# Optimization experiments

Hardware: AMD Instinct MI355X
Metric: run time of the kernel (lower is better)

The kernel has to match this reference:

```python
import jax, jax.numpy as jnp
import numpy as np

_J6 = jnp.array([[0,0,0,0,0,1],[0,0,0,0,-1,0],[0,0,0,1,0,0],
                 [0,0,1,0,0,0],[0,-1,0,0,0,0],[1,0,0,0,0,0]], dtype=jnp.float32)
_PAIRS4 = [(0,1),(0,2),(0,3),(1,2),(1,3),(2,3)]
H = 16  # n_heads

def _ln(x, g, b, eps=1e-5):
    m = jnp.mean(x, axis=-1, keepdims=True)
    v = jnp.var(x, axis=-1, keepdims=True)
    return (x - m) / jnp.sqrt(v + eps) * g + b

def _exterior(p1, p2):
    # Plucker coordinates of the line through p1,p2 in R^4 -> R^6, normalized
    parts = [p1[..., i] * p2[..., j] - p1[..., j] * p2[..., i] for i, j in _PAIRS4]
    L = jnp.stack(parts, axis=-1)
    n = jnp.linalg.norm(L, axis=-1, keepdims=True)
    return L / jnp.maximum(n, 1e-12)

def _iterated_gram_attn(x, Wqkv, bqkv, W1w, W2w, W1r, W2r, Wmv, bmv, Wmg, bmg,
                        mem_scale, iter_mix, decay_logits, Wout, bout):
    B, T, D = x.shape
    dh = D // H
    # ---- standard causal attention branch ----
    qkv = (x @ Wqkv + bqkv).reshape(B, T, 3, H, dh)
    q = jnp.transpose(qkv[:, :, 0], (0, 2, 1, 3))  # bhtd
    k = jnp.transpose(qkv[:, :, 1], (0, 2, 1, 3))
    v = jnp.transpose(qkv[:, :, 2], (0, 2, 1, 3))
    scores = jnp.einsum('bhtd,bhsd->bhts', q, k) * (dh ** -0.5)
    causal = jnp.tril(jnp.ones((T, T), dtype=bool))
    scores = jnp.where(causal, scores, -jnp.inf)
    attn = jax.nn.softmax(scores, axis=-1)  # dropout is eval-mode identity
    seq_out = jnp.einsum('bhts,bhsd->bhtd', attn, v).transpose(0, 2, 1, 3).reshape(B, T, D)
    # ---- Gram memory branch ----
    x_prev = jnp.concatenate([jnp.zeros_like(x[:, :1]), x[:, :-1]], axis=1)
    w1 = (x_prev @ W1w).reshape(B, T, H, 4)
    w2 = (x @ W2w).reshape(B, T, H, 4)
    write_lines = _exterior(w1, w2)                       # (B,T,H,6)
    r1 = (x @ W1r).reshape(B, T, H, 4)
    r2 = (x @ W2r).reshape(B, T, H, 4)
    read_lines = _exterior(r1, r2)                        # (B,T,H,6)
    Jw = jnp.einsum('bthi,ij->bhtj', write_lines, _J6)    # (B,H,T,6)
    rd = jnp.transpose(read_lines, (0, 2, 1, 3))          # (B,H,T,6)
    decays = jax.nn.sigmoid(decay_logits)                 # (H,)
    pos = jnp.arange(T, dtype=x.dtype)
    outer = Jw[..., :, None] * Jw[..., None, :]           # (B,H,T,6,6)
    dinv = (1.0 / jnp.maximum(decays, 1e-6))[:, None] ** pos[None, :]  # (H,T)
    M = jnp.cumsum(outer * dinv[None, :, :, None, None], axis=2)
    M = jnp.concatenate([jnp.zeros_like(M[:, :, :1]), M[:, :, :-1]], axis=2)  # shift: strictly past
    dfwd = decays[:, None] ** pos[None, :]
    M = M * dfwd[None, :, :, None, None]                  # (B,H,T,6,6)
    rdM = jnp.einsum('bhti,bhtij->bhtj', rd, M)
    score_M = jnp.sum(rdM * rd, axis=-1)                  # (B,H,T)
    score_M2 = jnp.sum(rdM * rdM, axis=-1)
    alpha = jax.nn.sigmoid(iter_mix[0])
    mem_score = (1 - alpha) * score_M + alpha * score_M2
    mem_val = x @ Wmv + bmv                               # (B,T,D)
    gate = jax.nn.sigmoid(x @ Wmg + bmg)                  # (B,T,H)
    gated = jax.nn.sigmoid(jnp.transpose(mem_score, (0, 2, 1)) * mem_scale[None, None, :]) * gate
    gated = jnp.mean(gated, axis=-1, keepdims=True)       # (B,T,1)
    return (seq_out + gated * mem_val) @ Wout + bout

def _block(x, ln1_g, ln1_b, Wqkv, bqkv, W1w, W2w, W1r, W2r, Wmv, bmv, Wmg, bmg,
           mem_scale, iter_mix, decay_logits, Wout, bout,
           ln2_g, ln2_b, Wfc, bfc, Wproj, bproj):
    h = _ln(x, ln1_g, ln1_b)
    x = x + _iterated_gram_attn(h, Wqkv, bqkv, W1w, W2w, W1r, W2r, Wmv, bmv,
                                Wmg, bmg, mem_scale, iter_mix, decay_logits, Wout, bout)
    h2 = _ln(x, ln2_g, ln2_b)
    mlp = jax.nn.gelu(h2 @ Wfc + bfc, approximate=False) @ Wproj + bproj
    return x + mlp

def setup_inputs() -> dict:
    key = jax.random.key(0)
    B, T, D = 2, 1024, 1024
    dff = 4 * D
    ks = jax.random.split(key, 16)
    s = 0.02
    inp = {
        'x': jax.random.normal(ks[0], (B, T, D), jnp.float32),
        'ln1_g': jnp.ones((D,), jnp.float32), 'ln1_b': jnp.zeros((D,), jnp.float32),
        'Wqkv': jax.random.normal(ks[1], (D, 3 * D), jnp.float32) * s,
        'bqkv': jnp.zeros((3 * D,), jnp.float32),
        'W1w': jax.random.normal(ks[2], (D, 4 * H), jnp.float32) * s,
        'W2w': jax.random.normal(ks[3], (D, 4 * H), jnp.float32) * s,
        'W1r': jax.random.normal(ks[4], (D, 4 * H), jnp.float32) * s,
        'W2r': jax.random.normal(ks[5], (D, 4 * H), jnp.float32) * s,
        'Wmv': jax.random.normal(ks[6], (D, D), jnp.float32) * s,
        'bmv': jnp.zeros((D,), jnp.float32),
        'Wmg': jax.random.normal(ks[7], (D, H), jnp.float32) * s,
        'bmg': jnp.zeros((H,), jnp.float32),
        'mem_scale': jnp.full((H,), 0.1, jnp.float32),
        'iter_mix': jnp.zeros((1,), jnp.float32),
        'decay_logits': jnp.full((H,), 4.6, jnp.float32) + 0.1 * jax.random.normal(ks[8], (H,), jnp.float32),
        'Wout': jax.random.normal(ks[9], (D, D), jnp.float32) * s,
        'bout': jnp.zeros((D,), jnp.float32),
        'ln2_g': jnp.ones((D,), jnp.float32), 'ln2_b': jnp.zeros((D,), jnp.float32),
        'Wfc': jax.random.normal(ks[10], (D, dff), jnp.float32) * s,
        'bfc': jnp.zeros((dff,), jnp.float32),
        'Wproj': jax.random.normal(ks[11], (dff, D), jnp.float32) * s,
        'bproj': jnp.zeros((D,), jnp.float32),
    }
    return inp

def reference(x, ln1_g, ln1_b, Wqkv, bqkv, W1w, W2w, W1r, W2r, Wmv, bmv, Wmg, bmg,
              mem_scale, iter_mix, decay_logits, Wout, bout,
              ln2_g, ln2_b, Wfc, bfc, Wproj, bproj):
    return _block(x, ln1_g, ln1_b, Wqkv, bqkv, W1w, W2w, W1r, W2r, Wmv, bmv, Wmg, bmg,
                  mem_scale, iter_mix, decay_logits, Wout, bout,
                  ln2_g, ln2_b, Wfc, bfc, Wproj, bproj)
```

## Files before the change

### kernel.cpp

```cpp
#include <hip/hip_runtime.h>
#include <hip/hip_bf16.h>
#include <math.h>

typedef float f32x4 __attribute__((ext_vector_type(4)));
typedef _Float16 f16x8 __attribute__((ext_vector_type(8)));
typedef _Float16 f16x4 __attribute__((ext_vector_type(4)));

#define TT 1024
#define DD 1024
#define QS 4608

typedef __attribute__((address_space(1))) const void gas_void;
typedef __attribute__((address_space(3))) void las_void;
static __device__ __forceinline__ void gl_lds16(const void* g, void* l) {
  __builtin_amdgcn_global_load_lds((gas_void*)g, (las_void*)l, 16, 0, 0);
}

__global__ __launch_bounds__(512) void gemm_t16(
    const _Float16* __restrict__ A, const _Float16* __restrict__ Wt,
    const float* __restrict__ bias, void* __restrict__ Cv,
    int N, int K, int act, int gx, int mode, int ktiles) {
  __shared__ __align__(16) _Float16 As[3][128 * 32];
  __shared__ __align__(16) _Float16 Bs[3][128 * 32];
  const int tid = threadIdx.x;
  const int lane = tid & 63;
  const int wid = tid >> 6;
  const int wr = wid >> 1, wc = wid & 1;
  const int g = lane >> 4, l16 = lane & 15;
  const int cpx = gridDim.x >> 3;
  const int wg = (blockIdx.x & 7) * cpx + (blockIdx.x >> 3);
  const int row0 = (wg / gx) * 128, col0 = (wg % gx) * 128;
  const int kbeg = blockIdx.y * ktiles * 32;

  f32x4 acc[2][4];
#pragma unroll
  for (int m = 0; m < 2; ++m)
#pragma unroll
    for (int n = 0; n < 4; ++n) acc[m][n] = (f32x4){0.f, 0.f, 0.f, 0.f};

  const int srow = tid >> 2;
  const int goff = ((tid & 3) ^ ((srow >> 1) & 3)) << 3;
  const _Float16* agp = A + (size_t)(row0 + srow) * K + kbeg + goff;
  const _Float16* bgp = Wt + (size_t)(col0 + srow) * K + kbeg + goff;
  const int ldst = tid * 16;

  const int prm = (l16 >> 1) & 3;

  gl_lds16(agp, (char*)As[0] + ldst);
  gl_lds16(bgp, (char*)Bs[0] + ldst);
  if (1 < ktiles) {
    gl_lds16(agp + 32, (char*)As[1] + ldst);
    gl_lds16(bgp + 32, (char*)Bs[1] + ldst);
  }

  int cs = 0, ss = 2;
  for (int kt = 0; kt < ktiles; ++kt) {
    if (kt < ktiles - 1) asm volatile("s_waitcnt vmcnt(2)" ::: "memory");
    else                 asm volatile("s_waitcnt vmcnt(0)" ::: "memory");
    __builtin_amdgcn_s_barrier();
    __builtin_amdgcn_sched_barrier(0);
    if (kt + 2 < ktiles) {
      const int kp = (kt + 2) * 32;
      gl_lds16(agp + kp, (char*)As[ss] + ldst);
      gl_lds16(bgp + kp, (char*)Bs[ss] + ldst);
    }
    f16x8 af[2], bf[4];
#pragma unroll
    for (int m = 0; m < 2; ++m) {
      const int r = wr * 32 + m * 16 + l16;
      af[m] = *(const f16x8*)(As[cs] + r * 32 + ((g ^ prm) << 3));
    }
#pragma unroll
    for (int n = 0; n < 4; ++n) {
      const int r = wc * 64 + n * 16 + l16;
      bf[n] = *(const f16x8*)(Bs[cs] + r * 32 + ((g ^ prm) << 3));
    }
#pragma unroll
    for (int m = 0; m < 2; ++m)
#pragma unroll
      for (int n = 0; n < 4; ++n)
        acc[m][n] = __builtin_amdgcn_mfma_f32_16x16x32_f16(af[m], bf[n], acc[m][n], 0, 0, 0);
    cs = (cs == 2) ? 0 : cs + 1;
    ss = (ss == 2) ? 0 : ss + 1;
  }
#pragma unroll
  for (int m = 0; m < 2; ++m) {
#pragma unroll
    for (int n = 0; n < 4; ++n) {
      const int col = col0 + wc * 64 + n * 16 + l16;
      const float bv = (mode != 2 && bias) ? bias[col] : 0.f;
#pragma unroll
      for (int rg = 0; rg < 4; ++rg) {
        const int row = row0 + wr * 32 + m * 16 + g * 4 + rg;
        const size_t off = (size_t)row * N + col;
        float v = acc[m][n][rg] + bv;
        if (act == 1) v = 0.5f * v * (1.f + erff(v * 0.70710678118654752f));
        if (mode == 2) atomicAdd(&((float*)Cv)[off], v);
        else ((_Float16*)Cv)[off] = (_Float16)v;
      }
    }
  }
}

__global__ __launch_bounds__(256) void transT(const float* __restrict__ W,
                                              _Float16* __restrict__ WT, int K, int N) {
  __shared__ float tile[64][65];
  const int n0 = blockIdx.x * 64, k0 = blockIdx.y * 64;
  const int tn = threadIdx.x & 63, tk4 = threadIdx.x >> 6;
#pragma unroll
  for (int it = 0; it < 16; ++it) {
    const int k = k0 + it * 4 + tk4;
    tile[tn][it * 4 + tk4] = W[(size_t)k * N + n0 + tn];
  }
  __syncthreads();
  const int on = threadIdx.x >> 2, ok = threadIdx.x & 3;
  f16x8 a, b;
#pragma unroll
  for (int j = 0; j < 8; ++j) {
    a[j] = (_Float16)tile[on][ok * 16 + j];
    b[j] = (_Float16)tile[on][ok * 16 + 8 + j];
  }
  _Float16* dst = WT + (size_t)(n0 + on) * K + k0 + ok * 16;
  *(f16x8*)dst = a;
  *(f16x8*)(dst + 8) = b;
}

__global__ __launch_bounds__(256) void prep_megaT(
    const float* __restrict__ Wqkv, const float* __restrict__ W1w, const float* __restrict__ W2w,
    const float* __restrict__ W1r, const float* __restrict__ W2r, const float* __restrict__ Wmg,
    const float* __restrict__ Wmv, _Float16* __restrict__ WmT) {
  __shared__ float tile[64][65];
  const int n0 = blockIdx.x * 64, k0 = blockIdx.y * 64;
  const int tn = threadIdx.x & 63, tk4 = threadIdx.x >> 6;
#pragma unroll
  for (int it = 0; it < 16; ++it) {
    const int k = k0 + it * 4 + tk4;
    const int n = n0 + tn;
    float v;
    if (n < 3072) v = Wqkv[(size_t)k * 3072 + n];
    else if (n < 3136) v = W1w[k * 64 + n - 3072];
    else if (n < 3200) v = W2w[k * 64 + n - 3136];
    else if (n < 3264) v = W1r[k * 64 + n - 3200];
    else if (n < 3328) v = W2r[k * 64 + n - 3264];
    else if (n < 3344) v = Wmg[k * 16 + n - 3328];
    else if (n < 3584) v = 0.f;
    else v = Wmv[(size_t)k * 1024 + n - 3584];
    tile[tn][it * 4 + tk4] = v;
  }
  __syncthreads();
  const int on = threadIdx.x >> 2, ok = threadIdx.x & 3;
  f16x8 a, b;
#pragma unroll
  for (int j = 0; j < 8; ++j) {
    a[j] = (_Float16)tile[on][ok * 16 + j];
    b[j] = (_Float16)tile[on][ok * 16 + 8 + j];
  }
  _Float16* dst = WmT + (size_t)(n0 + on) * 1024 + k0 + ok * 16;
  *(f16x8*)dst = a;
  *(f16x8*)(dst + 8) = b;
}

__global__ void bm_init(const float* __restrict__ bqkv, const float* __restrict__ bmg,
                        const float* __restrict__ bmv, float* __restrict__ bm) {
  const int col = blockIdx.x * 256 + threadIdx.x;
  if (col >= 4608) return;
  float b = 0.f;
  if (col < 3072) b = bqkv[col];
  else if (col >= 3328 && col < 3344) b = bmg[col - 3328];
  else if (col >= 3584) b = bmv[col - 3584];
  bm[col] = b;
}

__global__ __launch_bounds__(256) void ln16(const float* __restrict__ in,
    const float* __restrict__ gw, const float* __restrict__ bw, _Float16* __restrict__ out) {
  const int row = blockIdx.x, tid = threadIdx.x;
  const float* x = in + (size_t)row * DD;
  const float4 v = *(const float4*)(x + tid * 4);
  float s = v.x + v.y + v.z + v.w;
  float sq = v.x * v.x + v.y * v.y + v.z * v.z + v.w * v.w;
#pragma unroll
  for (int off = 32; off >= 1; off >>= 1) { s += __shfl_xor(s, off); sq += __shfl_xor(sq, off); }
  __shared__ float red[8];
  const int lane = tid & 63, wv = tid >> 6;
  if (lane == 0) { red[wv] = s; red[4 + wv] = sq; }
  __syncthreads();
  s = red[0] + red[1] + red[2] + red[3];
  sq = red[4] + red[5] + red[6] + red[7];
  const float mean = s * (1.f / 1024.f);
  const float var = sq * (1.f / 1024.f) - mean * mean;
  const float rstd = rsqrtf(var + 1e-5f);
  const float4 g4 = *(const float4*)(gw + tid * 4);
  const float4 b4 = *(const float4*)(bw + tid * 4);
  f16x4 o;
  o[0] = (_Float16)((v.x - mean) * rstd * g4.x + b4.x);
  o[1] = (_Float16)((v.y - mean) * rstd * g4.y + b4.y);
  o[2] = (_Float16)((v.z - mean) * rstd * g4.z + b4.z);
  o[3] = (_Float16)((v.w - mean) * rstd * g4.w + b4.w);
  *(f16x4*)(out + (size_t)row * DD + tid * 4) = o;
}

static __device__ __forceinline__ int swzA(int row, int k) {
  return row * 64 + ((((k >> 3) ^ row) & 7) << 3) + (k & 7);
}
static __device__ __forceinline__ int swzV(int row, int k) {
  return row * 64 + ((((k >> 3) ^ row ^ (row >> 3)) & 7) << 3) + (k & 7);
}

__global__ __launch_bounds__(256) void attn_mfma(const _Float16* __restrict__ qkv,
                                                 _Float16* __restrict__ seq_out) {
  __shared__ __align__(16) _Float16 Kl[64 * 64];
  __shared__ __align__(16) _Float16 Vt[64 * 64];
  __shared__ __align__(16) _Float16 Pl[4][16 * 64];
  const int tid = threadIdx.x, lane = tid & 63, wq = tid >> 6;
  const int g = lane >> 4, l16 = lane & 15;
  const int qt = blockIdx.x, hh = blockIdx.y, bb = blockIdx.z;
  const int nt = qt + 1;

  f16x8 qf[2];
  {
    const _Float16* qp = qkv + (size_t)(bb * TT + qt * 64 + wq * 16 + l16) * QS + hh * 64;
#pragma unroll
    for (int ks = 0; ks < 2; ++ks) {
      const f16x8 a = *(const f16x8*)(qp + ks * 32 + g * 8);
#pragma unroll
      for (int j = 0; j < 8; ++j) qf[ks][j] = (_Float16)((float)a[j] * 0.125f);
    }
  }

  f32x4 oacc[4];
#pragma unroll
  for (int n = 0; n < 4; ++n) oacc[n] = (f32x4){0.f, 0.f, 0.f, 0.f};
  float m[4] = {-INFINITY, -INFINITY, -INFINITY, -INFINITY};
  float l[4] = {0.f, 0.f, 0.f, 0.f};

  const int skey = tid >> 2, sc4 = tid & 3;

  for (int tt = 0; tt < nt; ++tt) {
    if (tt) __syncthreads();
    {
      const _Float16* kp = qkv + (size_t)(bb * TT + tt * 64 + skey) * QS + hh * 64 + 1024;
      const _Float16* vp = kp + 1024;
#pragma unroll
      for (int ii = 0; ii < 4; ++ii) {
        const int d0 = sc4 * 4 + ii * 16;
        *(f16x4*)(Kl + swzA(skey, d0)) = *(const f16x4*)(kp + d0);
        const f16x4 vv = *(const f16x4*)(vp + d0);
        Vt[swzV(d0 + 0, skey)] = vv[0];
        Vt[swzV(d0 + 1, skey)] = vv[1];
        Vt[swzV(d0 + 2, skey)] = vv[2];
        Vt[swzV(d0 + 3, skey)] = vv[3];
      }
    }
    __syncthreads();
    f32x4 s[4];
#pragma unroll
    for (int n = 0; n < 4; ++n) s[n] = (f32x4){0.f, 0.f, 0.f, 0.f};
#pragma unroll
    for (int ks = 0; ks < 2; ++ks) {
      f16x8 kf[4];
#pragma unroll
      for (int n = 0; n < 4; ++n) kf[n] = *(const f16x8*)(Kl + swzA(n * 16 + l16, ks * 32 + g * 8));
#pragma unroll
      for (int n = 0; n < 4; ++n)
        s[n] = __builtin_amdgcn_mfma_f32_16x16x32_f16(qf[ks], kf[n], s[n], 0, 0, 0);
    }
    if (tt == qt) {
      const int rloc = wq * 16 + g * 4;
#pragma unroll
      for (int n = 0; n < 4; ++n) {
        const int cloc = n * 16 + l16;
#pragma unroll
        for (int reg = 0; reg < 4; ++reg)
          if (cloc > rloc + reg) s[n][reg] = -INFINITY;
      }
    }
    float f[4];
#pragma unroll
    for (int reg = 0; reg < 4; ++reg) {
      float t = fmaxf(fmaxf(s[0][reg], s[1][reg]), fmaxf(s[2][reg], s[3][reg]));
#pragma unroll
      for (int off = 1; off < 16; off <<= 1) t = fmaxf(t, __shfl_xor(t, off));
      const float nm = fmaxf(m[reg], t);
      f[reg] = __expf(m[reg] - nm);
      m[reg] = nm;
    }
    float rs[4] = {0.f, 0.f, 0.f, 0.f};
#pragma unroll
    for (int n = 0; n < 4; ++n) {
#pragma unroll
      for (int reg = 0; reg < 4; ++reg) {
        const float p = __expf(s[n][reg] - m[reg]);
        rs[reg] += p;
        Pl[wq][swzA(g * 4 + reg, n * 16 + l16)] = (_Float16)p;
      }
    }
#pragma unroll
    for (int reg = 0; reg < 4; ++reg) {
      float t = rs[reg];
#pragma unroll
      for (int off = 1; off < 16; off <<= 1) t += __shfl_xor(t, off);
      l[reg] = l[reg] * f[reg] + t;
    }
#pragma unroll
    for (int n = 0; n < 4; ++n)
#pragma unroll
      for (int reg = 0; reg < 4; ++reg) oacc[n][reg] *= f[reg];
#pragma unroll
    for (int ks = 0; ks < 2; ++ks) {
      const f16x8 pa = *(const f16x8*)(Pl[wq] + swzA(l16, ks * 32 + g * 8));
      f16x8 vb[4];
#pragma unroll
      for (int n = 0; n < 4; ++n) vb[n] = *(const f16x8*)(Vt + swzV(n * 16 + l16, ks * 32 + g * 8));
#pragma unroll
      for (int n = 0; n < 4; ++n)
        oacc[n] = __builtin_amdgcn_mfma_f32_16x16x32_f16(pa, vb[n], oacc[n], 0, 0, 0);
    }
  }
#pragma unroll
  for (int n = 0; n < 4; ++n) {
#pragma unroll
    for (int reg = 0; reg < 4; ++reg) {
      const int r = qt * 64 + wq * 16 + g * 4 + reg;
      seq_out[(size_t)(bb * TT + r) * DD + hh * 64 + n * 16 + l16] = (_Float16)(oacc[n][reg] / l[reg]);
    }
  }
}

static __device__ __forceinline__ void ext6(const float* a, const float* b, float* L) {
  L[0] = a[0] * b[1] - a[1] * b[0];
  L[1] = a[0] * b[2] - a[2] * b[0];
  L[2] = a[0] * b[3] - a[3] * b[0];
  L[3] = a[1] * b[2] - a[2] * b[1];
  L[4] = a[1] * b[3] - a[3] * b[1];
  L[5] = a[2] * b[3] - a[3] * b[2];
  const float n = sqrtf(L[0]*L[0] + L[1]*L[1] + L[2]*L[2] + L[3]*L[3] + L[4]*L[4] + L[5]*L[5]);
  const float s = 1.f / fmaxf(n, 1e-12f);
#pragma unroll
  for (int i = 0; i < 6; ++i) L[i] *= s;
}

__global__ void lines_post(const _Float16* __restrict__ mega, float* __restrict__ jw,
                           float* __restrict__ rdv, float* __restrict__ gate) {
  const int idx = blockIdx.x * 256 + threadIdx.x;
  const int h = idx & 15;
  const int bt = idx >> 4;
  const int t = bt & 1023;
  const int b = bt >> 10;
  const _Float16* row = mega + (size_t)bt * QS + 3072;
  float w1[4] = {0.f, 0.f, 0.f, 0.f}, w2[4], r1[4], r2[4];
  if (t > 0) {
#pragma unroll
    for (int i = 0; i < 4; ++i) w1[i] = (float)row[-QS + h * 4 + i];
  }
#pragma unroll
  for (int i = 0; i < 4; ++i) {
    w2[i] = (float)row[64 + h * 4 + i];
    r1[i] = (float)row[128 + h * 4 + i];
    r2[i] = (float)row[192 + h * 4 + i];
  }
  const float gp = (float)row[256 + h];
  float wl[6], rl[6];
  ext6(w1, w2, wl);
  ext6(r1, r2, rl);
  const size_t o = ((size_t)(b * 16 + h) * 1024 + t) * 6;
  jw[o + 0] =  wl[5]; jw[o + 1] = -wl[4]; jw[o + 2] =  wl[3];
  jw[o + 3] =  wl[2]; jw[o + 4] = -wl[1]; jw[o + 5] =  wl[0];
#pragma unroll
  for (int i = 0; i < 6; ++i) rdv[o + i] = rl[i];
  gate[idx] = 1.f / (1.f + __expf(-gp));
}

static __device__ __forceinline__ int midx(int i, int j) {
  return (i <= j) ? (i * (13 - i)) / 2 + (j - i) : (j * (13 - j)) / 2 + (i - j);
}

__global__ __launch_bounds__(64) void gram_scan(const float* __restrict__ jwv,
    const float* __restrict__ rdv, const float* __restrict__ decay_logits,
    const float* __restrict__ iter_mix, float* __restrict__ mem_score) {
  const int h = blockIdx.x & 15, b = blockIdx.x >> 4;
  const int lane = threadIdx.x;
  const float decay = 1.f / (1.f + __expf(-decay_logits[h]));
  const float alpha = 1.f / (1.f + __expf(-iter_mix[0]));
  __shared__ float sd[64 * 193];
  const size_t base = (size_t)(b * 16 + h) * 1024 * 6;
  for (int it = 0; it < 96; ++it) {
    const int idx = it * 64 + lane;
    const int t = idx / 6, i = idx - 6 * t;
    const int ld = t >> 4, s = t & 15;
    sd[ld * 193 + s * 6 + i] = jwv[base + idx];
    sd[ld * 193 + 96 + s * 6 + i] = rdv[base + idx];
  }
  __syncthreads();
  const float* seg = sd + lane * 193;

  float C[21];
#pragma unroll
  for (int e = 0; e < 21; ++e) C[e] = 0.f;
  for (int s = 0; s < 16; ++s) {
    float J[6], dJ[6];
#pragma unroll
    for (int i = 0; i < 6; ++i) { J[i] = seg[s * 6 + i]; dJ[i] = decay * J[i]; }
#pragma unroll
    for (int i = 0; i < 6; ++i)
#pragma unroll
      for (int j = i; j < 6; ++j)
        C[midx(i, j)] = decay * C[midx(i, j)] + dJ[i] * J[j];
  }
  const float d2 = decay * decay, d4 = d2 * d2, d8 = d4 * d4;
  float fk = d8 * d8;
#pragma unroll
  for (int k = 0; k < 6; ++k) {
    const int off = 1 << k;
#pragma unroll
    for (int e = 0; e < 21; ++e) {
      const float u = __shfl(C[e], lane - off);
      if (lane >= off) C[e] += fk * u;
    }
    fk = fk * fk;
  }
  float M[21];
#pragma unroll
  for (int e = 0; e < 21; ++e) {
    const float u = __shfl(C[e], lane - 1);
    M[e] = (lane >= 1) ? u : 0.f;
  }
  float* msp = mem_score + (size_t)(b * 16 + h) * 1024 + lane * 16;
  for (int s = 0; s < 16; ++s) {
    float J[6], r[6];
#pragma unroll
    for (int i = 0; i < 6; ++i) { J[i] = seg[s * 6 + i]; r[i] = seg[96 + s * 6 + i]; }
    float rdM[6];
#pragma unroll
    for (int i = 0; i < 6; ++i) {
      float a = 0.f;
#pragma unroll
      for (int j = 0; j < 6; ++j) a += M[midx(i, j)] * r[j];
      rdM[i] = a;
    }
    float s1 = 0.f, s2 = 0.f;
#pragma unroll
    for (int i = 0; i < 6; ++i) { s1 += rdM[i] * r[i]; s2 += rdM[i] * rdM[i]; }
    msp[s] = (1.f - alpha) * s1 + alpha * s2;
    float dJ[6];
#pragma unroll
    for (int i = 0; i < 6; ++i) dJ[i] = decay * J[i];
#pragma unroll
    for (int i = 0; i < 6; ++i)
#pragma unroll
      for (int j = i; j < 6; ++j)
        M[midx(i, j)] = decay * M[midx(i, j)] + dJ[i] * J[j];
  }
}

__global__ __launch_bounds__(256) void combine_kernel(const _Float16* __restrict__ seq,
    const _Float16* __restrict__ mega, const float* __restrict__ ms,
    const float* __restrict__ gate, const float* __restrict__ mem_scale,
    _Float16* __restrict__ outp) {
  const int bt = blockIdx.x;
  const int b = bt >> 10, t = bt & 1023;
  __shared__ float hterm[16];
  const int tid = threadIdx.x;
  if (tid < 16) {
    const float sc = ms[(size_t)(b * 16 + tid) * 1024 + t];
    const float gt = gate[(size_t)bt * 16 + tid];
    hterm[tid] = (1.f / (1.f + __expf(-sc * mem_scale[tid]))) * gt;
  }
  __syncthreads();
  float acc = 0.f;
#pragma unroll
  for (int h = 0; h < 16; ++h) acc += hterm[h];
  const float g = acc * (1.f / 16.f);
  const f16x4 s4 = *(const f16x4*)(seq + (size_t)bt * 1024 + tid * 4);
  const f16x4 m4 = *(const f16x4*)(mega + (size_t)bt * QS + 3584 + tid * 4);
  f16x4 o;
#pragma unroll
  for (int j = 0; j < 4; ++j) o[j] = (_Float16)((float)s4[j] + g * (float)m4[j]);
  *(f16x4*)(outp + (size_t)bt * 1024 + tid * 4) = o;
}

__global__ void addb_init(const float* __restrict__ src, const float* __restrict__ bias,
                          float* __restrict__ dst) {
  const size_t i = (size_t)blockIdx.x * 256 + threadIdx.x;
  const int c4 = (int)(i & 255);
  const float4 s = ((const float4*)src)[i];
  const float4 b = ((const float4*)bias)[c4];
  float4 o;
  o.x = s.x + b.x; o.y = s.y + b.y; o.z = s.z + b.z; o.w = s.w + b.w;
  ((float4*)dst)[i] = o;
}

extern "C" void kernel_launch(void* const* d_in, const int* in_sizes, int n_in,
                              void* d_out, int out_size, void* d_ws, size_t ws_size,
                              hipStream_t stream) {
  (void)in_sizes; (void)n_in; (void)out_size; (void)ws_size;
  const float* x       = (const float*)d_in[0];
  const float* ln1_g   = (const float*)d_in[1];
  const float* ln1_b   = (const float*)d_in[2];
  const float* Wqkv    = (const float*)d_in[3];
  const float* bqkv    = (const float*)d_in[4];
  const float* W1w     = (const float*)d_in[5];
  const float* W2w     = (const float*)d_in[6];
  const float* W1r     = (const float*)d_in[7];
  const float* W2r     = (const float*)d_in[8];
  const float* Wmv     = (const float*)d_in[9];
  const float* bmv     = (const float*)d_in[10];
  const float* Wmg     = (const float*)d_in[11];
  const float* bmg     = (const float*)d_in[12];
  const float* mscale  = (const float*)d_in[13];
  const float* itermix = (const float*)d_in[14];
  const float* dlogits = (const float*)d_in[15];
  const float* Wout    = (const float*)d_in[16];
  const float* bout    = (const float*)d_in[17];
  const float* ln2_g   = (const float*)d_in[18];
  const float* ln2_b   = (const float*)d_in[19];
  const float* Wfc     = (const float*)d_in[20];
  const float* bfc     = (const float*)d_in[21];
  const float* Wproj   = (const float*)d_in[22];
  const float* bproj   = (const float*)d_in[23];
  float* out = (float*)d_out;
  float* ws = (float*)d_ws;

  const size_t M1 = 1u << 20;
  _Float16* h16    = (_Float16*)ws;
  _Float16* WmT    = (_Float16*)(ws + 1 * M1);
  float*    bm     = ws + 3407872;
  float*    jw     = ws + 3538944;
  float*    rd     = ws + 3538944 + 196608;
  float*    gate   = ws + 3538944 + 393216;
  float*    ms     = ws + 3538944 + 425984;
  float*    y      = ws + 4 * M1;
  _Float16* mega   = (_Float16*)(ws + 6 * M1);
  _Float16* fc16   = (_Float16*)(ws + 6 * M1);
  _Float16* seq16  = (_Float16*)(ws + 11010048);
  _Float16* WoutT  = (_Float16*)(ws + 12058624);
  _Float16* WfcT   = (_Float16*)(ws + 12 * M1);
  _Float16* WprojT = (_Float16*)(ws + 14 * M1);

  prep_megaT<<<dim3(72, 16), 256, 0, stream>>>(Wqkv, W1w, W2w, W1r, W2r, Wmg, Wmv, WmT);
  bm_init<<<18, 256, 0, stream>>>(bqkv, bmg, bmv, bm);
  transT<<<dim3(16, 16), 256, 0, stream>>>(Wout, WoutT, 1024, 1024);
  transT<<<dim3(64, 16), 256, 0, stream>>>(Wfc, WfcT, 1024, 4096);
  transT<<<dim3(16, 64), 256, 0, stream>>>(Wproj, WprojT, 4096, 1024);

  ln16<<<2048, 256, 0, stream>>>(x, ln1_g, ln1_b, h16);
  gemm_t16<<<576, 512, 0, stream>>>(h16, WmT, bm, mega, 4608, 1024, 0, 36, 1, 32);
  attn_mfma<<<dim3(16, 16, 2), 256, 0, stream>>>(mega, seq16);
  lines_post<<<128, 256, 0, stream>>>(mega, jw, rd, gate);
  gram_scan<<<32, 64, 0, stream>>>(jw, rd, dlogits, itermix, ms);
  combine_kernel<<<2048, 256, 0, stream>>>(seq16, mega, ms, gate, mscale, h16);
  addb_init<<<2048, 256, 0, stream>>>(x, bout, y);
  gemm_t16<<<dim3(128, 4), 512, 0, stream>>>(h16, WoutT, nullptr, y, 1024, 1024, 0, 8, 2, 8);
  ln16<<<2048, 256, 0, stream>>>(y, ln2_g, ln2_b, h16);
  gemm_t16<<<512, 512, 0, stream>>>(h16, WfcT, bfc, fc16, 4096, 1024, 1, 32, 1, 32);
  addb_init<<<2048, 256, 0, stream>>>(y, bproj, out);
  gemm_t16<<<dim3(128, 4), 512, 0, stream>>>(fc16, WprojT, nullptr, out, 1024, 4096, 0, 8, 2, 32);
}
```

Baseline: 251.0 us.

## Merge weight-prep kernels, pair causal attention tiles, fuse residual into Wout GEMM

All weight transposes and the bias init are merged into a single prep_all launch, which cuts launch overhead. The attention kernel now gives each block two query tiles (p and 15-p) that share the K/V loads in shared memory, so per-block causal work is balanced and K/V traffic is reduced. The Wout projection no longer uses a split-K atomicAdd with a separate addb_init. It runs as one full-K GEMM with a mode that adds bias and residual in the epilogue and writes fp32 directly. In exchange the Wout GEMM has fewer blocks (128), and the attention grid is halved while each block does roughly twice the work.

```diff
diff --git a/kernel.cpp b/kernel.cpp
--- a/kernel.cpp
+++ b/kernel.cpp
@@ -18,10 +18,10 @@
 
 __global__ __launch_bounds__(512) void gemm_t16(
     const _Float16* __restrict__ A, const _Float16* __restrict__ Wt,
-    const float* __restrict__ bias, void* __restrict__ Cv,
-    int N, int K, int act, int gx, int mode, int ktiles) {
-  __shared__ __align__(16) _Float16 As[3][128 * 32];
-  __shared__ __align__(16) _Float16 Bs[3][128 * 32];
+    const float* __restrict__ bias, const float* __restrict__ residual,
+    void* __restrict__ Cv, int N, int K, int act, int gx, int mode, int ktiles) {
+  __shared__ __align__(16) _Float16 As[3][4096];
+  __shared__ __align__(16) _Float16 Bs[3][4096];
   const int tid = threadIdx.x;
   const int lane = tid & 63;
   const int wid = tid >> 6;
@@ -72,8 +72,8 @@
     }
 #pragma unroll
     for (int n = 0; n < 4; ++n) {
-      const int r = wc * 64 + n * 16 + l16;
-      bf[n] = *(const f16x8*)(Bs[cs] + r * 32 + ((g ^ prm) << 3));
+      const int c = wc * 64 + n * 16 + l16;
+      bf[n] = *(const f16x8*)(Bs[cs] + c * 32 + ((g ^ prm) << 3));
     }
 #pragma unroll
     for (int m = 0; m < 2; ++m)
@@ -96,24 +96,24 @@
         float v = acc[m][n][rg] + bv;
         if (act == 1) v = 0.5f * v * (1.f + erff(v * 0.70710678118654752f));
         if (mode == 2) atomicAdd(&((float*)Cv)[off], v);
+        else if (mode == 3) ((float*)Cv)[off] = v + residual[off];
         else ((_Float16*)Cv)[off] = (_Float16)v;
       }
     }
   }
 }
 
-__global__ __launch_bounds__(256) void transT(const float* __restrict__ W,
-                                              _Float16* __restrict__ WT, int K, int N) {
+static __device__ __forceinline__ void trans_tile(const float* __restrict__ W,
+    _Float16* __restrict__ WT, int K, int N, int n0, int k0, int tid) {
   __shared__ float tile[64][65];
-  const int n0 = blockIdx.x * 64, k0 = blockIdx.y * 64;
-  const int tn = threadIdx.x & 63, tk4 = threadIdx.x >> 6;
+  const int tn = tid & 63, tk4 = tid >> 6;
 #pragma unroll
   for (int it = 0; it < 16; ++it) {
     const int k = k0 + it * 4 + tk4;
     tile[tn][it * 4 + tk4] = W[(size_t)k * N + n0 + tn];
   }
   __syncthreads();
-  const int on = threadIdx.x >> 2, ok = threadIdx.x & 3;
+  const int on = tid >> 2, ok = tid & 3;
   f16x8 a, b;
 #pragma unroll
   for (int j = 0; j < 8; ++j) {
@@ -125,50 +125,64 @@
   *(f16x8*)(dst + 8) = b;
 }
 
-__global__ __launch_bounds__(256) void prep_megaT(
+__global__ __launch_bounds__(256) void prep_all(
     const float* __restrict__ Wqkv, const float* __restrict__ W1w, const float* __restrict__ W2w,
     const float* __restrict__ W1r, const float* __restrict__ W2r, const float* __restrict__ Wmg,
-    const float* __restrict__ Wmv, _Float16* __restrict__ WmT) {
-  __shared__ float tile[64][65];
-  const int n0 = blockIdx.x * 64, k0 = blockIdx.y * 64;
-  const int tn = threadIdx.x & 63, tk4 = threadIdx.x >> 6;
-#pragma unroll
-  for (int it = 0; it < 16; ++it) {
-    const int k = k0 + it * 4 + tk4;
-    const int n = n0 + tn;
-    float v;
-    if (n < 3072) v = Wqkv[(size_t)k * 3072 + n];
-    else if (n < 3136) v = W1w[k * 64 + n - 3072];
-    else if (n < 3200) v = W2w[k * 64 + n - 3136];
-    else if (n < 3264) v = W1r[k * 64 + n - 3200];
-    else if (n < 3328) v = W2r[k * 64 + n - 3264];
-    else if (n < 3344) v = Wmg[k * 16 + n - 3328];
-    else if (n < 3584) v = 0.f;
-    else v = Wmv[(size_t)k * 1024 + n - 3584];
-    tile[tn][it * 4 + tk4] = v;
-  }
-  __syncthreads();
-  const int on = threadIdx.x >> 2, ok = threadIdx.x & 3;
-  f16x8 a, b;
-#pragma unroll
-  for (int j = 0; j < 8; ++j) {
-    a[j] = (_Float16)tile[on][ok * 16 + j];
-    b[j] = (_Float16)tile[on][ok * 16 + 8 + j];
-  }
-  _Float16* dst = WmT + (size_t)(n0 + on) * 1024 + k0 + ok * 16;
-  *(f16x8*)dst = a;
-  *(f16x8*)(dst + 8) = b;
-}
-
-__global__ void bm_init(const float* __restrict__ bqkv, const float* __restrict__ bmg,
-                        const float* __restrict__ bmv, float* __restrict__ bm) {
-  const int col = blockIdx.x * 256 + threadIdx.x;
-  if (col >= 4608) return;
-  float b = 0.f;
-  if (col < 3072) b = bqkv[col];
-  else if (col >= 3328 && col < 3344) b = bmg[col - 3328];
-  else if (col >= 3584) b = bmv[col - 3584];
-  bm[col] = b;
+    const float* __restrict__ Wmv, const float* __restrict__ Wout, const float* __restrict__ Wfc,
+    const float* __restrict__ Wproj, const float* __restrict__ bqkv, const float* __restrict__ bmg,
+    const float* __restrict__ bmv, _Float16* __restrict__ WmT, _Float16* __restrict__ WoutT,
+    _Float16* __restrict__ WfcT, _Float16* __restrict__ WprojT, float* __restrict__ bm) {
+  const int id = blockIdx.x;
+  const int tid = threadIdx.x;
+  if (id < 1152) {
+    __shared__ float tile[64][65];
+    const int n0 = (id % 72) * 64, k0 = (id / 72) * 64;
+    const int tn = tid & 63, tk4 = tid >> 6;
+#pragma unroll
+    for (int it = 0; it < 16; ++it) {
+      const int k = k0 + it * 4 + tk4;
+      const int n = n0 + tn;
+      float v;
+      if (n < 3072) v = Wqkv[(size_t)k * 3072 + n];
+      else if (n < 3136) v = W1w[k * 64 + n - 3072];
+      else if (n < 3200) v = W2w[k * 64 + n - 3136];
+      else if (n < 3264) v = W1r[k * 64 + n - 3200];
+      else if (n < 3328) v = W2r[k * 64 + n - 3264];
+      else if (n < 3344) v = Wmg[k * 16 + n - 3328];
+      else if (n < 3584) v = 0.f;
+      else v = Wmv[(size_t)k * 1024 + n - 3584];
+      tile[tn][it * 4 + tk4] = v;
+    }
+    __syncthreads();
+    const int on = tid >> 2, ok = tid & 3;
+    f16x8 a, b;
+#pragma unroll
+    for (int j = 0; j < 8; ++j) {
+      a[j] = (_Float16)tile[on][ok * 16 + j];
+      b[j] = (_Float16)tile[on][ok * 16 + 8 + j];
+    }
+    _Float16* dst = WmT + (size_t)(n0 + on) * 1024 + k0 + ok * 16;
+    *(f16x8*)dst = a;
+    *(f16x8*)(dst + 8) = b;
+  } else if (id < 1408) {
+    const int i2 = id - 1152;
+    trans_tile(Wout, WoutT, 1024, 1024, (i2 % 16) * 64, (i2 / 16) * 64, tid);
+  } else if (id < 2432) {
+    const int i2 = id - 1408;
+    trans_tile(Wfc, WfcT, 1024, 4096, (i2 % 64) * 64, (i2 / 64) * 64, tid);
+  } else if (id < 3456) {
+    const int i2 = id - 2432;
+    trans_tile(Wproj, WprojT, 4096, 1024, (i2 % 16) * 64, (i2 / 16) * 64, tid);
+  } else {
+    const int col = (id - 3456) * 256 + tid;
+    if (col < 4608) {
+      float b = 0.f;
+      if (col < 3072) b = bqkv[col];
+      else if (col >= 3328 && col < 3344) b = bmg[col - 3328];
+      else if (col >= 3584) b = bmv[col - 3584];
+      bm[col] = b;
+    }
+  }
 }
 
 __global__ __launch_bounds__(256) void ln16(const float* __restrict__ in,
@@ -206,6 +220,75 @@
   return row * 64 + ((((k >> 3) ^ row ^ (row >> 3)) & 7) << 3) + (k & 7);
 }
 
+static __device__ __forceinline__ void attn_step(
+    const f16x8* qf, f32x4* oacc, float* m, float* l,
+    const _Float16* Kl, const _Float16* Vt, _Float16* Plw,
+    bool diag, int wq, int g, int l16) {
+  f32x4 s[4];
+#pragma unroll
+  for (int n = 0; n < 4; ++n) s[n] = (f32x4){0.f, 0.f, 0.f, 0.f};
+#pragma unroll
+  for (int ks = 0; ks < 2; ++ks) {
+    f16x8 kf[4];
+#pragma unroll
+    for (int n = 0; n < 4; ++n) kf[n] = *(const f16x8*)(Kl + swzA(n * 16 + l16, ks * 32 + g * 8));
+#pragma unroll
+    for (int n = 0; n < 4; ++n)
+      s[n] = __builtin_amdgcn_mfma_f32_16x16x32_f16(qf[ks], kf[n], s[n], 0, 0, 0);
+  }
+  if (diag) {
+    const int rloc = wq * 16 + g * 4;
+#pragma unroll
+    for (int n = 0; n < 4; ++n) {
+      const int cloc = n * 16 + l16;
+#pragma unroll
+      for (int reg = 0; reg < 4; ++reg)
+        if (cloc > rloc + reg) s[n][reg] = -INFINITY;
+    }
+  }
+  float f[4];
+#pragma unroll
+  for (int reg = 0; reg < 4; ++reg) {
+    float t = fmaxf(fmaxf(s[0][reg], s[1][reg]), fmaxf(s[2][reg], s[3][reg]));
+#pragma unroll
+    for (int off = 1; off < 16; off <<= 1) t = fmaxf(t, __shfl_xor(t, off));
+    const float nm = fmaxf(m[reg], t);
+    f[reg] = __expf(m[reg] - nm);
+    m[reg] = nm;
+  }
+  float rs[4] = {0.f, 0.f, 0.f, 0.f};
+#pragma unroll
+  for (int n = 0; n < 4; ++n) {
+#pragma unroll
+    for (int reg = 0; reg < 4; ++reg) {
+      const float p = __expf(s[n][reg] - m[reg]);
+      rs[reg] += p;
+      Plw[swzA(g * 4 + reg, n * 16 + l16)] = (_Float16)p;
+    }
+  }
+#pragma unroll
+  for (int reg = 0; reg < 4; ++reg) {
+    float t = rs[reg];
+#pragma unroll
+    for (int off = 1; off < 16; off <<= 1) t += __shfl_xor(t, off);
+    l[reg] = l[reg] * f[reg] + t;
+  }
+#pragma unroll
+  for (int n = 0; n < 4; ++n)
+#pragma unroll
+    for (int reg = 0; reg < 4; ++reg) oacc[n][reg] *= f[reg];
+#pragma unroll
+  for (int ks = 0; ks < 2; ++ks) {
+    const f16x8 pa = *(const f16x8*)(Plw + swzA(l16, ks * 32 + g * 8));
+    f16x8 vb[4];
+#pragma unroll
+    for (int n = 0; n < 4; ++n) vb[n] = *(const f16x8*)(Vt + swzV(n * 16 + l16, ks * 32 + g * 8));
+#pragma unroll
+    for (int n = 0; n < 4; ++n)
+      oacc[n] = __builtin_amdgcn_mfma_f32_16x16x32_f16(pa, vb[n], oacc[n], 0, 0, 0);
+  }
+}
+
 __global__ __launch_bounds__(256) void attn_mfma(const _Float16* __restrict__ qkv,
                                                  _Float16* __restrict__ seq_out) {
   __shared__ __align__(16) _Float16 Kl[64 * 64];
@@ -213,29 +296,40 @@
   __shared__ __align__(16) _Float16 Pl[4][16 * 64];
   const int tid = threadIdx.x, lane = tid & 63, wq = tid >> 6;
   const int g = lane >> 4, l16 = lane & 15;
-  const int qt = blockIdx.x, hh = blockIdx.y, bb = blockIdx.z;
-  const int nt = qt + 1;
-
-  f16x8 qf[2];
+  const int p = blockIdx.x, hh = blockIdx.y, bb = blockIdx.z;
+  const int qt0 = p, qt1 = 15 - p;
+  const int ntt = qt1 + 1;
+
+  f16x8 qf0[2], qf1[2];
   {
-    const _Float16* qp = qkv + (size_t)(bb * TT + qt * 64 + wq * 16 + l16) * QS + hh * 64;
+    const _Float16* q0 = qkv + (size_t)(bb * TT + qt0 * 64 + wq * 16 + l16) * QS + hh * 64;
+    const _Float16* q1 = qkv + (size_t)(bb * TT + qt1 * 64 + wq * 16 + l16) * QS + hh * 64;
 #pragma unroll
     for (int ks = 0; ks < 2; ++ks) {
-      const f16x8 a = *(const f16x8*)(qp + ks * 32 + g * 8);
-#pragma unroll
-      for (int j = 0; j < 8; ++j) qf[ks][j] = (_Float16)((float)a[j] * 0.125f);
-    }
-  }
-
-  f32x4 oacc[4];
-#pragma unroll
-  for (int n = 0; n < 4; ++n) oacc[n] = (f32x4){0.f, 0.f, 0.f, 0.f};
-  float m[4] = {-INFINITY, -INFINITY, -INFINITY, -INFINITY};
-  float l[4] = {0.f, 0.f, 0.f, 0.f};
+      const f16x8 a0 = *(const f16x8*)(q0 + ks * 32 + g * 8);
+      const f16x8 a1 = *(const f16x8*)(q1 + ks * 32 + g * 8);
+#pragma unroll
+      for (int j = 0; j < 8; ++j) {
+        qf0[ks][j] = (_Float16)((float)a0[j] * 0.125f);
+        qf1[ks][j] = (_Float16)((float)a1[j] * 0.125f);
+      }
+    }
+  }
+
+  f32x4 oacc0[4], oacc1[4];
+#pragma unroll
+  for (int n = 0; n < 4; ++n) {
+    oacc0[n] = (f32x4){0.f, 0.f, 0.f, 0.f};
+    oacc1[n] = (f32x4){0.f, 0.f, 0.f, 0.f};
+  }
+  float m0[4] = {-INFINITY, -INFINITY, -INFINITY, -INFINITY};
+  float l0[4] = {0.f, 0.f, 0.f, 0.f};
+  float m1[4] = {-INFINITY, -INFINITY, -INFINITY, -INFINITY};
+  float l1[4] = {0.f, 0.f, 0.f, 0.f};
 
   const int skey = tid >> 2, sc4 = tid & 3;
 
-  for (int tt = 0; tt < nt; ++tt) {
+  for (int tt = 0; tt < ntt; ++tt) {
     if (tt) __syncthreads();
     {
       const _Float16* kp = qkv + (size_t)(bb * TT + tt * 64 + skey) * QS + hh * 64 + 1024;
@@ -252,76 +346,18 @@
       }
     }
     __syncthreads();
-    f32x4 s[4];
-#pragma unroll
-    for (int n = 0; n < 4; ++n) s[n] = (f32x4){0.f, 0.f, 0.f, 0.f};
-#pragma unroll
-    for (int ks = 0; ks < 2; ++ks) {
-      f16x8 kf[4];
-#pragma unroll
-      for (int n = 0; n < 4; ++n) kf[n] = *(const f16x8*)(Kl + swzA(n * 16 + l16, ks * 32 + g * 8));
-#pragma unroll
-      for (int n = 0; n < 4; ++n)
-        s[n] = __builtin_amdgcn_mfma_f32_16x16x32_f16(qf[ks], kf[n], s[n], 0, 0, 0);
-    }
-    if (tt == qt) {
-      const int rloc = wq * 16 + g * 4;
-#pragma unroll
-      for (int n = 0; n < 4; ++n) {
-        const int cloc = n * 16 + l16;
-#pragma unroll
-        for (int reg = 0; reg < 4; ++reg)
-          if (cloc > rloc + reg) s[n][reg] = -INFINITY;
-      }
-    }
-    float f[4];
+    attn_step(qf1, oacc1, m1, l1, Kl, Vt, Pl[wq], tt == qt1, wq, g, l16);
+    if (tt <= qt0)
+      attn_step(qf0, oacc0, m0, l0, Kl, Vt, Pl[wq], tt == qt0, wq, g, l16);
+  }
+#pragma unroll
+  for (int n = 0; n < 4; ++n) {
 #pragma unroll
     for (int reg = 0; reg < 4; ++reg) {
-      float t = fmaxf(fmaxf(s[0][reg], s[1][reg]), fmaxf(s[2][reg], s[3][reg]));
-#pragma unroll
-      for (int off = 1; off < 16; off <<= 1) t = fmaxf(t, __shfl_xor(t, off));
-      const float nm = fmaxf(m[reg], t);
-      f[reg] = __expf(m[reg] - nm);
-      m[reg] = nm;
-    }
-    float rs[4] = {0.f, 0.f, 0.f, 0.f};
-#pragma unroll
-    for (int n = 0; n < 4; ++n) {
-#pragma unroll
-      for (int reg = 0; reg < 4; ++reg) {
-        const float p = __expf(s[n][reg] - m[reg]);
-        rs[reg] += p;
-        Pl[wq][swzA(g * 4 + reg, n * 16 + l16)] = (_Float16)p;
-      }
-    }
-#pragma unroll
-    for (int reg = 0; reg < 4; ++reg) {
-      float t = rs[reg];
-#pragma unroll
-      for (int off = 1; off < 16; off <<= 1) t += __shfl_xor(t, off);
-      l[reg] = l[reg] * f[reg] + t;
-    }
-#pragma unroll
-    for (int n = 0; n < 4; ++n)
-#pragma unroll
-      for (int reg = 0; reg < 4; ++reg) oacc[n][reg] *= f[reg];
-#pragma unroll
-    for (int ks = 0; ks < 2; ++ks) {
-      const f16x8 pa = *(const f16x8*)(Pl[wq] + swzA(l16, ks * 32 + g * 8));
-      f16x8 vb[4];
-#pragma unroll
-      for (int n = 0; n < 4; ++n) vb[n] = *(const f16x8*)(Vt + swzV(n * 16 + l16, ks * 32 + g * 8));
-#pragma unroll
-      for (int n = 0; n < 4; ++n)
-        oacc[n] = __builtin_amdgcn_mfma_f32_16x16x32_f16(pa, vb[n], oacc[n], 0, 0, 0);
-    }
-  }
-#pragma unroll
-  for (int n = 0; n < 4; ++n) {
-#pragma unroll
-    for (int reg = 0; reg < 4; ++reg) {
-      const int r = qt * 64 + wq * 16 + g * 4 + reg;
-      seq_out[(size_t)(bb * TT + r) * DD + hh * 64 + n * 16 + l16] = (_Float16)(oacc[n][reg] / l[reg]);
+      const int r0 = qt0 * 64 + wq * 16 + g * 4 + reg;
+      const int r1 = qt1 * 64 + wq * 16 + g * 4 + reg;
+      seq_out[(size_t)(bb * TT + r0) * DD + hh * 64 + n * 16 + l16] = (_Float16)(oacc0[n][reg] / l0[reg]);
+      seq_out[(size_t)(bb * TT + r1) * DD + hh * 64 + n * 16 + l16] = (_Float16)(oacc1[n][reg] / l1[reg]);
     }
   }
 }
@@ -536,22 +572,18 @@
   _Float16* WfcT   = (_Float16*)(ws + 12 * M1);
   _Float16* WprojT = (_Float16*)(ws + 14 * M1);
 
-  prep_megaT<<<dim3(72, 16), 256, 0, stream>>>(Wqkv, W1w, W2w, W1r, W2r, Wmg, Wmv, WmT);
-  bm_init<<<18, 256, 0, stream>>>(bqkv, bmg, bmv, bm);
-  transT<<<dim3(16, 16), 256, 0, stream>>>(Wout, WoutT, 1024, 1024);
-  transT<<<dim3(64, 16), 256, 0, stream>>>(Wfc, WfcT, 1024, 4096);
-  transT<<<dim3(16, 64), 256, 0, stream>>>(Wproj, WprojT, 4096, 1024);
+  prep_all<<<3474, 256, 0, stream>>>(Wqkv, W1w, W2w, W1r, W2r, Wmg, Wmv, Wout, Wfc, Wproj,
+                                     bqkv, bmg, bmv, WmT, WoutT, WfcT, WprojT, bm);
 
   ln16<<<2048, 256, 0, stream>>>(x, ln1_g, ln1_b, h16);
-  gemm_t16<<<576, 512, 0, stream>>>(h16, WmT, bm, mega, 4608, 1024, 0, 36, 1, 32);
-  attn_mfma<<<dim3(16, 16, 2), 256, 0, stream>>>(mega, seq16);
+  gemm_t16<<<576, 512, 0, stream>>>(h16, WmT, bm, nullptr, mega, 4608, 1024, 0, 36, 1, 32);
+  attn_mfma<<<dim3(8, 16, 2), 256, 0, stream>>>(mega, seq16);
   lines_post<<<128, 256, 0, stream>>>(mega, jw, rd, gate);
   gram_scan<<<32, 64, 0, stream>>>(jw, rd, dlogits, itermix, ms);
   combine_kernel<<<2048, 256, 0, stream>>>(seq16, mega, ms, gate, mscale, h16);
-  addb_init<<<2048, 256, 0, stream>>>(x, bout, y);
-  gemm_t16<<<dim3(128, 4), 512, 0, stream>>>(h16, WoutT, nullptr, y, 1024, 1024, 0, 8, 2, 8);
+  gemm_t16<<<128, 512, 0, stream>>>(h16, WoutT, bout, x, y, 1024, 1024, 0, 8, 3, 32);
   ln16<<<2048, 256, 0, stream>>>(y, ln2_g, ln2_b, h16);
-  gemm_t16<<<512, 512, 0, stream>>>(h16, WfcT, bfc, fc16, 4096, 1024, 1, 32, 1, 32);
+  gemm_t16<<<512, 512, 0, stream>>>(h16, WfcT, bfc, nullptr, fc16, 4096, 1024, 1, 32, 1, 32);
   addb_init<<<2048, 256, 0, stream>>>(y, bproj, out);
-  gemm_t16<<<dim3(128, 4), 512, 0, stream>>>(fc16, WprojT, nullptr, out, 1024, 4096, 0, 8, 2, 32);
-}
+  gemm_t16<<<dim3(128, 4), 512, 0, stream>>>(fc16, WprojT, nullptr, nullptr, out, 1024, 4096, 0, 8, 2, 32);
+}
```

Result: faster. 235.9 us (median of 3 runs) (-6.0%).
